# Optimization experiments

Hardware: AMD Instinct MI355X
Metric: run time of the kernel (lower is better)

The kernel has to match this reference:

```python
import jax, jax.numpy as jnp
import numpy as np

FS = 512.0
T = 2048
CYC_PHA, CYC_AMP = 3, 6
NBINS = 18
PHA_BANDS = [(2.0 + 2.0 * k, 4.0 + 2.0 * k) for k in range(10)]
AMP_BANDS = [(30.0 + 12.0 * k, 42.0 + 12.0 * k) for k in range(10)]


def _design_filter(fs, low, high, cycle):
    # windowed-sinc bandpass, taps = cycle * fs / low (tensorpac cycle rule), forced odd
    n = int(cycle * fs / low)
    if n % 2 == 0:
        n += 1
    t = np.arange(n) - (n - 1) / 2.0
    lp = lambda fc: 2.0 * fc / fs * np.sinc(2.0 * fc / fs * t)
    h = (lp(high) - lp(low)) * np.hamming(n)
    fc = 0.5 * (low + high)
    h = h / np.abs(np.sum(h * np.exp(-2j * np.pi * fc / fs * t)))  # unit gain at band center
    return h.astype(np.float32)


def _build_kernels():
    filts = [_design_filter(FS, l, h, CYC_PHA) for l, h in PHA_BANDS] + \
            [_design_filter(FS, l, h, CYC_AMP) for l, h in AMP_BANDS]
    L = max(f.shape[0] for f in filts)
    padded = []
    for f in filts:
        p = L - f.shape[0]
        pl = p // 2
        padded.append(np.pad(f, (pl, p - pl)))
    return np.stack(padded)  # (F, L), L odd


def _conv_same(sig, kernels):
    # sig: (N, Tp), kernels: (F, L) -> (N, F, Tp); cross-correlation, 'same' padding (L odd)
    L = kernels.shape[1]
    pad = (L - 1) // 2
    return jax.lax.conv_general_dilated(
        sig[:, None, :], kernels[:, None, :], window_strides=(1,),
        padding=((pad, L - 1 - pad),), dimension_numbers=("NCH", "OIH", "NCH"))


def _analytic(x):
    # FFT-based Hilbert analytic signal along last axis
    n = x.shape[-1]
    h = np.zeros(n, np.float32)
    h[0] = 1.0
    if n % 2 == 0:
        h[n // 2] = 1.0
        h[1:n // 2] = 2.0
    else:
        h[1:(n + 1) // 2] = 2.0
    return jnp.fft.ifft(jnp.fft.fft(x, axis=-1) * h, axis=-1)


def _modulation_index(pha, amp):
    # Tort MI: pha (B,C,P,S,T), amp (B,C,A,S,T) -> (B,C,P,A)
    idx = jnp.clip(jnp.floor((pha + jnp.pi) / (2.0 * jnp.pi) * NBINS), 0, NBINS - 1).astype(jnp.int32)
    sums, cnts = [], []
    for b in range(NBINS):  # fixed small bin count
        m = (idx == b).astype(amp.dtype)                       # (B,C,P,S,T)
        sums.append(jnp.einsum('bcpst,bcast->bcpas', m, amp))  # (B,C,P,A,S)
        cnts.append(m.sum(-1))                                 # (B,C,P,S)
    amp_sum = jnp.stack(sums, -1)                              # (B,C,P,A,S,N)
    cnt = jnp.stack(cnts, -1)[:, :, :, None, :, :]             # (B,C,P,1,S,N)
    amp_mean = amp_sum / jnp.maximum(cnt, 1.0)
    p = amp_mean / jnp.maximum(amp_mean.sum(-1, keepdims=True), 1e-12)
    log_n = jnp.log(jnp.asarray(NBINS, amp.dtype))
    mi = (log_n + (p * jnp.log(jnp.maximum(p, 1e-12))).sum(-1)) / log_n
    return mi.mean(-1)  # average over segments


def setup_inputs() -> dict:
    key = jax.random.key(0)
    x = jax.random.normal(key, (4, 8, 4, T), dtype=jnp.float32)
    kernels = jnp.asarray(_build_kernels())
    return {"x": x, "kernels": kernels}


def reference(x, kernels):
    B, C, S, Tlen = x.shape
    npha = len(PHA_BANDS)
    pad = kernels.shape[1] - 1  # max_padlen (edge_mode)
    sig = x.reshape(B * C * S, Tlen)
    sig = jnp.pad(sig, ((0, 0), (pad, pad)), mode='reflect')
    # filtfilt_mode: average forward conv and time-reversed conv
    fwd = _conv_same(sig, kernels)
    bwd = _conv_same(sig[:, ::-1], kernels)[:, :, ::-1]
    filt = 0.5 * (fwd + bwd)
    filt = filt[:, :, pad:-pad]  # strip edge padding -> (N, F, T)
    ana = _analytic(filt)
    pha = jnp.arctan2(ana.imag[:, :npha], ana.real[:, :npha])
    amp = jnp.sqrt(ana.real[:, npha:] ** 2 + ana.imag[:, npha:] ** 2)
    pha = pha.reshape(B, C, npha, S, Tlen)
    amp = amp.reshape(B, C, len(AMP_BANDS), S, Tlen)
    return _modulation_index(pha, amp)
```

## Files before the change

kernel.cpp:

```cpp
#include <hip/hip_runtime.h>
#include <math.h>

#define TT 2048
#define LK 769
#define NF 20
#define NS 128
#define NB 18

typedef __attribute__((ext_vector_type(8))) short short8;
typedef __attribute__((ext_vector_type(4))) float f32x4;

__global__ __launch_bounds__(256) void convhil_kernel(const float* __restrict__ x,
                                                      const float* __restrict__ ker,
                                                      float* __restrict__ filt) {
  __shared__ __align__(16) float smem[4400];
  __shared__ int red[4][4];
  __shared__ __align__(16) float2 tw[TT];
  float* w   = smem;
  float* hs1 = smem + 2832;
  float* hs2 = smem + 3616;
  float2* z  = (float2*)smem;
  const int tid = threadIdx.x;
  const int ord = blockIdx.x;
  const int p = ord / NS;
  const int n = ord % NS;
  const int o1 = p;
  const int o2 = 10 + (9 - p);
  const float* xr = x + n * TT;
  for (int j = tid; j < 2832; j += 256) {
    float v = 0.f;
    if (j < 2816) {
      int m = j - 384;
      if (m < 0) m = -m;
      if (m > 2047) m = 4094 - m;
      v = xr[m];
    }
    w[j] = v;
  }
  for (int i = tid; i < TT; i += 256) {
    if (i == 0) { tw[0] = make_float2(1.f, 0.f); }
    else {
      int half = 1 << (31 - __clz(i));
      int j = i - half;
      float ang = -3.14159265358979323846f * (float)j / (float)half;
      float s, c;
      sincosf(ang, &s, &c);
      tw[i] = make_float2(c, s);
    }
  }
  const float* kr1 = ker + o1 * LK;
  const float* kr2 = ker + o2 * LK;
  int k0 = 784, k1 = 0, m0 = 784, m1 = 0;
  for (int k = tid; k < 784; k += 256) {
    float v1 = 0.f, v2 = 0.f;
    if (k < LK) {
      v1 = 0.5f * (kr1[k] + kr1[LK - 1 - k]);
      v2 = 0.5f * (kr2[k] + kr2[LK - 1 - k]);
    }
    hs1[k] = v1;
    hs2[k] = v2;
    if (v1 != 0.f) { k0 = min(k0, k); k1 = max(k1, k + 1); }
    if (v2 != 0.f) { m0 = min(m0, k); m1 = max(m1, k + 1); }
  }
#pragma unroll
  for (int off = 32; off > 0; off >>= 1) {
    k0 = min(k0, __shfl_down(k0, off));
    k1 = max(k1, __shfl_down(k1, off));
    m0 = min(m0, __shfl_down(m0, off));
    m1 = max(m1, __shfl_down(m1, off));
  }
  const int wid = tid >> 6;
  if ((tid & 63) == 0) { red[wid][0] = k0; red[wid][1] = k1; red[wid][2] = m0; red[wid][3] = m1; }
  __syncthreads();
  k0 = min(min(red[0][0], red[1][0]), min(red[2][0], red[3][0]));
  k1 = max(max(red[0][1], red[1][1]), max(red[2][1], red[3][1]));
  m0 = min(min(red[0][2], red[1][2]), min(red[2][2], red[3][2]));
  m1 = max(max(red[0][3], red[1][3]), max(red[2][3], red[3][3]));
  const int A0 = __builtin_amdgcn_readfirstlane(k0 & ~7);
  const int A1 = __builtin_amdgcn_readfirstlane((k1 + 7) & ~7);
  const int B0 = __builtin_amdgcn_readfirstlane(m0 & ~7);
  const int B1 = __builtin_amdgcn_readfirstlane((m1 + 7) & ~7);
  const int U0 = min(A0, B0);
  const int U1 = max(A1, B1);

  const int bA = 4 * tid;
  const int bB = 1024 + 4 * tid;
  float acc1A[4], acc1B[4], acc2A[4], acc2B[4];
#pragma unroll
  for (int r = 0; r < 4; ++r) { acc1A[r] = 0.f; acc1B[r] = 0.f; acc2A[r] = 0.f; acc2B[r] = 0.f; }
  if (U0 < U1) {
    float4 a0 = *(const float4*)&w[bA + U0];
    float4 a1 = *(const float4*)&w[bA + U0 + 4];
    float4 a2 = *(const float4*)&w[bA + U0 + 8];
    float4 b0 = *(const float4*)&w[bB + U0];
    float4 b1 = *(const float4*)&w[bB + U0 + 4];
    float4 b2 = *(const float4*)&w[bB + U0 + 8];
    float4 h1a = *(const float4*)&hs1[U0];
    float4 h1b = *(const float4*)&hs1[U0 + 4];
    float4 h2a = *(const float4*)&hs2[U0];
    float4 h2b = *(const float4*)&hs2[U0 + 4];
    for (int k = U0; k < U1; k += 8) {
      float4 a3 = *(const float4*)&w[bA + k + 12];
      float4 a4 = *(const float4*)&w[bA + k + 16];
      float4 b3 = *(const float4*)&w[bB + k + 12];
      float4 b4 = *(const float4*)&w[bB + k + 16];
      float4 h1an = *(const float4*)&hs1[k + 8];
      float4 h1bn = *(const float4*)&hs1[k + 12];
      float4 h2an = *(const float4*)&hs2[k + 8];
      float4 h2bn = *(const float4*)&hs2[k + 12];
      float wa[11] = {a0.x, a0.y, a0.z, a0.w, a1.x, a1.y, a1.z, a1.w,
                      a2.x, a2.y, a2.z};
      float wb[11] = {b0.x, b0.y, b0.z, b0.w, b1.x, b1.y, b1.z, b1.w,
                      b2.x, b2.y, b2.z};
      float h1[8] = {h1a.x, h1a.y, h1a.z, h1a.w, h1b.x, h1b.y, h1b.z, h1b.w};
      float h2[8] = {h2a.x, h2a.y, h2a.z, h2a.w, h2b.x, h2b.y, h2b.z, h2b.w};
      if (k >= A0 && k < A1) {
#pragma unroll
        for (int r = 0; r < 4; ++r) {
#pragma unroll
          for (int j = 0; j < 8; ++j) {
            acc1A[r] = fmaf(h1[j], wa[r + j], acc1A[r]);
            acc1B[r] = fmaf(h1[j], wb[r + j], acc1B[r]);
          }
        }
      }
      if (k >= B0 && k < B1) {
#pragma unroll
        for (int r = 0; r < 4; ++r) {
#pragma unroll
          for (int j = 0; j < 8; ++j) {
            acc2A[r] = fmaf(h2[j], wa[r + j], acc2A[r]);
            acc2B[r] = fmaf(h2[j], wb[r + j], acc2B[r]);
          }
        }
      }
      a0 = a2; a1 = a3; a2 = a4;
      b0 = b2; b1 = b3; b2 = b4;
      h1a = h1an; h1b = h1bn;
      h2a = h2an; h2b = h2bn;
    }
  }
  __syncthreads();
#pragma unroll
  for (int r = 0; r < 4; ++r) {
    z[bA + r] = make_float2(acc1A[r], acc2A[r]);
    z[bB + r] = make_float2(acc1B[r], acc2B[r]);
  }
  __syncthreads();
  for (int bf = tid; bf < 1024; bf += 256) {
    const float2 t = tw[1024 + bf];
    const float2 u = z[bf];
    const float2 v = z[bf + 1024];
    z[bf] = make_float2(u.x + v.x, u.y + v.y);
    const float dr = u.x - v.x, di = u.y - v.y;
    z[bf + 1024] = make_float2(fmaf(t.x, dr, -(t.y * di)),
                               fmaf(t.x, di, t.y * dr));
  }
  __syncthreads();
  for (int Q = 256; Q >= 1; Q >>= 2) {
    for (int bf = tid; bf < 512; bf += 256) {
      const int j = bf & (Q - 1);
      const int base = ((bf & ~(Q - 1)) << 2) + j;
      const float2 x0 = z[base], x1 = z[base + Q];
      const float2 x2 = z[base + 2 * Q], x3 = z[base + 3 * Q];
      const float2 w1 = tw[2 * Q + j];
      const float2 w2 = tw[Q + j];
      const float w3r = w1.x * w2.x - w1.y * w2.y;
      const float w3i = w1.x * w2.y + w1.y * w2.x;
      const float t0r = x0.x + x2.x, t0i = x0.y + x2.y;
      const float t1r = x0.x - x2.x, t1i = x0.y - x2.y;
      const float t2r = x1.x + x3.x, t2i = x1.y + x3.y;
      const float t3r = x1.x - x3.x, t3i = x1.y - x3.y;
      z[base] = make_float2(t0r + t2r, t0i + t2i);
      const float a1r = t1r + t3i, a1i = t1i - t3r;
      z[base + Q] = make_float2(a1r * w1.x - a1i * w1.y,
                                a1r * w1.y + a1i * w1.x);
      const float a2r = t0r - t2r, a2i = t0i - t2i;
      z[base + 2 * Q] = make_float2(a2r * w2.x - a2i * w2.y,
                                    a2r * w2.y + a2i * w2.x);
      const float a3r = t1r - t3i, a3i = t1i + t3r;
      z[base + 3 * Q] = make_float2(a3r * w3r - a3i * w3i,
                                    a3r * w3i + a3i * w3r);
    }
    __syncthreads();
  }
  for (int pp = tid; pp < TT; pp += 256) {
    if (pp != 0 && pp != 2) {
      if (pp & 2) { z[pp] = make_float2(0.f, 0.f); }
      else        { float2 v = z[pp]; z[pp] = make_float2(2.f * v.x, 2.f * v.y); }
    }
  }
  __syncthreads();
  for (int Q = 1; Q <= 256; Q <<= 2) {
    for (int bf = tid; bf < 512; bf += 256) {
      const int j = bf & (Q - 1);
      const int base = ((bf & ~(Q - 1)) << 2) + j;
      const float2 y0 = z[base], y1 = z[base + Q];
      const float2 y2 = z[base + 2 * Q], y3 = z[base + 3 * Q];
      const float2 w1 = tw[2 * Q + j];
      const float2 w2 = tw[Q + j];
      const float w3r = w1.x * w2.x - w1.y * w2.y;
      const float w3i = w1.x * w2.y + w1.y * w2.x;
      const float u1r = y1.x * w1.x + y1.y * w1.y;
      const float u1i = y1.y * w1.x - y1.x * w1.y;
      const float u2r = y2.x * w2.x + y2.y * w2.y;
      const float u2i = y2.y * w2.x - y2.x * w2.y;
      const float u3r = y3.x * w3r + y3.y * w3i;
      const float u3i = y3.y * w3r - y3.x * w3i;
      const float t0r = y0.x + u2r, t0i = y0.y + u2i;
      const float t1r = y0.x - u2r, t1i = y0.y - u2i;
      const float t2r = u1r + u3r, t2i = u1i + u3i;
      const float t3r = u1r - u3r, t3i = u1i - u3i;
      z[base]         = make_float2(t0r + t2r, t0i + t2i);
      z[base + Q]     = make_float2(t1r - t3i, t1i + t3r);
      z[base + 2 * Q] = make_float2(t0r - t2r, t0i - t2i);
      z[base + 3 * Q] = make_float2(t1r + t3i, t1i - t3r);
    }
    __syncthreads();
  }
  for (int bf = tid; bf < 1024; bf += 256) {
    const float2 t = tw[1024 + bf];
    const float2 u = z[bf];
    const float2 v = z[bf + 1024];
    const float vr = v.x * t.x + v.y * t.y;
    const float vi = v.y * t.x - v.x * t.y;
    z[bf] = make_float2(u.x + vr, u.y + vi);
    z[bf + 1024] = make_float2(u.x - vr, u.y - vi);
  }
  __syncthreads();
  float* out1 = filt + ((size_t)n * NF + o1) * TT;
  float* out2 = filt + ((size_t)n * NF + o2) * TT;
  const float invN = 1.0f / 2048.0f;
  float phA[4], phB[4], amA[4], amB[4];
#pragma unroll
  for (int r = 0; r < 4; ++r) {
    float2 wvA = z[bA + r];
    float h1 = wvA.y * invN - acc2A[r];
    float h2 = acc1A[r] - wvA.x * invN;
    phA[r] = atan2f(h1, acc1A[r]);
    amA[r] = sqrtf(fmaf(acc2A[r], acc2A[r], h2 * h2));
    float2 wvB = z[bB + r];
    float g1 = wvB.y * invN - acc2B[r];
    float g2 = acc1B[r] - wvB.x * invN;
    phB[r] = atan2f(g1, acc1B[r]);
    amB[r] = sqrtf(fmaf(acc2B[r], acc2B[r], g2 * g2));
  }
  *(float4*)&out1[bA] = make_float4(phA[0], phA[1], phA[2], phA[3]);
  *(float4*)&out1[bB] = make_float4(phB[0], phB[1], phB[2], phB[3]);
  *(float4*)&out2[bA] = make_float4(amA[0], amA[1], amA[2], amA[3]);
  *(float4*)&out2[bB] = make_float4(amB[0], amB[1], amB[2], amB[3]);
}

__global__ __launch_bounds__(64) void mi_kernel(const float* __restrict__ filt,
                                                float* __restrict__ mi) {
  __shared__ __align__(16) unsigned int idx32[512];
  __shared__ float Cs[12][19];
  const int lane = threadIdx.x;
  const int blk = blockIdx.x;
  const int bc = blk / 40, jp = blk % 40;
  const float* ph = filt + ((size_t)(bc * 4 + jp / 10) * NF + (jp % 10)) * TT;
  for (int g = lane; g < 512; g += 64) {
    float4 v = *(const float4*)&ph[4 * g];
    float vv[4] = {v.x, v.y, v.z, v.w};
    unsigned int packed = 0;
#pragma unroll
    for (int j = 0; j < 4; ++j) {
      int b = (int)floorf((vv[j] + 3.14159274f) / 6.2831855f * 18.0f);
      b = b < 0 ? 0 : (b > 17 ? 17 : b);
      packed |= ((unsigned int)b) << (8 * j);
    }
    idx32[g] = packed;
  }
  __syncthreads();
  const int n16 = lane & 15;
  const int quad = lane >> 4;
  const int aband = n16 < 10 ? n16 : 9;
  const int ja = (jp & 3) + 4 * aband;
  const float* aptr = filt + ((size_t)(bc * 4 + ja / 10) * NF + 10 + (ja % 10)) * TT
                      + quad * 8;
  const bool isAmp = (n16 < 10);
  const bool isOne = (n16 == 10);
  f32x4 acc0 = {0.f, 0.f, 0.f, 0.f};
  f32x4 acc1 = {0.f, 0.f, 0.f, 0.f};
  float4 p0 = *(const float4*)(aptr);
  float4 p1 = *(const float4*)(aptr + 4);
  for (int s = 0; s < 64; ++s) {
    float4 c0 = p0, c1 = p1;
    if (s < 63) {
      p0 = *(const float4*)(aptr + (s + 1) * 32);
      p1 = *(const float4*)(aptr + (s + 1) * 32 + 4);
    }
    float a[8] = {c0.x, c0.y, c0.z, c0.w, c1.x, c1.y, c1.z, c1.w};
    short8 ah, am_, al;
#pragma unroll
    for (int j = 0; j < 8; ++j) {
      float v = isAmp ? a[j] : (isOne ? 1.0f : 0.0f);
      unsigned int u = __float_as_uint(v);
      float h = __uint_as_float(u & 0xFFFF0000u);
      float r1 = v - h;
      unsigned int u2 = __float_as_uint(r1);
      float md = __uint_as_float(u2 & 0xFFFF0000u);
      float r2 = r1 - md;
      unsigned int u3 = __float_as_uint(r2);
      ah[j] = (short)(u >> 16);
      am_[j] = (short)(u2 >> 16);
      al[j] = (short)(u3 >> 16);
    }
    const int dw = s * 8 + quad * 2;
    unsigned int d0 = idx32[dw], d1 = idx32[dw + 1];
    short8 b0, b1;
#pragma unroll
    for (int j = 0; j < 8; ++j) {
      unsigned int byte = ((j < 4 ? d0 : d1) >> ((j & 3) * 8)) & 0xFFu;
      b0[j] = (byte == (unsigned int)n16) ? (short)0x3F80 : (short)0;
      b1[j] = (byte == (unsigned int)(n16 + 16)) ? (short)0x3F80 : (short)0;
    }
    acc0 = __builtin_amdgcn_mfma_f32_16x16x32_bf16(ah, b0, acc0, 0, 0, 0);
    acc0 = __builtin_amdgcn_mfma_f32_16x16x32_bf16(am_, b0, acc0, 0, 0, 0);
    acc0 = __builtin_amdgcn_mfma_f32_16x16x32_bf16(al, b0, acc0, 0, 0, 0);
    acc1 = __builtin_amdgcn_mfma_f32_16x16x32_bf16(ah, b1, acc1, 0, 0, 0);
    acc1 = __builtin_amdgcn_mfma_f32_16x16x32_bf16(am_, b1, acc1, 0, 0, 0);
    acc1 = __builtin_amdgcn_mfma_f32_16x16x32_bf16(al, b1, acc1, 0, 0, 0);
  }
#pragma unroll
  for (int r = 0; r < 4; ++r) {
    int row = quad * 4 + r;
    if (row < 11) {
      Cs[row][n16] = acc0[r];
      if (n16 < 2) Cs[row][16 + n16] = acc1[r];
    }
  }
  __syncthreads();
  if (lane < 10) {
    float tot = 0.f, mb_[18];
#pragma unroll
    for (int b = 0; b < 18; ++b) {
      float mb = Cs[lane][b] / fmaxf(Cs[10][b], 1.0f);
      mb_[b] = mb; tot += mb;
    }
    tot = fmaxf(tot, 1e-12f);
    float s = 0.f;
#pragma unroll
    for (int b = 0; b < 18; ++b) {
      float pb = mb_[b] / tot;
      s += pb * logf(fmaxf(pb, 1e-12f));
    }
    const float LOGN = 2.8903717578961645f;
    mi[(size_t)blk * 10 + lane] = (LOGN + s) / LOGN;
  }
}

__global__ void out_kernel(const float* __restrict__ mi, float* __restrict__ out) {
  int i = blockIdx.x * 256 + threadIdx.x;
  if (i < 3200) {
    int a = i % 10, p = (i / 10) % 10, bc = i / 100;
    float s = 0.f;
    for (int sp = 0; sp < 4; ++sp)
      s += mi[((size_t)(bc * 40 + p * 4 + sp)) * 10 + a];
    out[i] = 0.25f * s;
  }
}

extern "C" void kernel_launch(void* const* d_in, const int* in_sizes, int n_in,
                              void* d_out, int out_size, void* d_ws, size_t ws_size,
                              hipStream_t stream) {
  (void)in_sizes; (void)n_in; (void)out_size; (void)ws_size;
  const float* x = (const float*)d_in[0];
  const float* ker = (const float*)d_in[1];
  float* out = (float*)d_out;
  float* filt = (float*)d_ws;
  float* mi = filt + (size_t)NS * NF * TT;

  convhil_kernel<<<NS * 10, 256, 0, stream>>>(x, ker, filt);
  mi_kernel<<<32 * 40, 64, 0, stream>>>(filt, mi);
  out_kernel<<<(3200 + 255) / 256, 256, 0, stream>>>(mi, out);
}
```

Baseline: 151.6 us.

## Precompute twiddles and symmetric filters once; split MI accumulation across four waves

A new prep kernel computes the FFT twiddle table, the symmetrized filter taps and their nonzero ranges once, instead of every convhil block redoing sincos, the filter folding and a block reduction. As a result convhil no longer holds the twiddle table in LDS, which frees about 16 KB of shared memory per block. It now reads twiddles from global memory, which adds global/L2 traffic inside the FFT. The MI kernel grows from one wave to four waves per block, each accumulating a quarter of the time segments, with partial histograms combined in LDS. The extra kernel launch adds a small fixed cost.

After: 139.4 us. 1.09x faster.

```diff
diff --git a/kernel.cpp b/kernel.cpp
--- a/kernel.cpp
+++ b/kernel.cpp
@@ -10,12 +10,56 @@
 typedef __attribute__((ext_vector_type(8))) short short8;
 typedef __attribute__((ext_vector_type(4))) float f32x4;
 
+__global__ __launch_bounds__(256) void prep_kernel(const float* __restrict__ ker,
+                                                   float2* __restrict__ tw,
+                                                   float* __restrict__ hsym,
+                                                   int* __restrict__ rng) {
+  __shared__ int red[4][2];
+  const int blk = blockIdx.x;
+  const int tid = threadIdx.x;
+  if (blk < 8) {
+    int i = blk * 256 + tid;
+    if (i == 0) { tw[0] = make_float2(1.f, 0.f); }
+    else {
+      int half = 1 << (31 - __clz(i));
+      int j = i - half;
+      float ang = -3.14159265358979323846f * (float)j / (float)half;
+      float s, c;
+      sincosf(ang, &s, &c);
+      tw[i] = make_float2(c, s);
+    }
+    return;
+  }
+  const int o = blk - 8;
+  const float* kr = ker + o * LK;
+  int k0 = 784, k1 = 0;
+  for (int k = tid; k < 784; k += 256) {
+    float v = 0.f;
+    if (k < LK) v = 0.5f * (kr[k] + kr[LK - 1 - k]);
+    hsym[o * 784 + k] = v;
+    if (v != 0.f) { k0 = min(k0, k); k1 = max(k1, k + 1); }
+  }
+#pragma unroll
+  for (int off = 32; off > 0; off >>= 1) {
+    k0 = min(k0, __shfl_down(k0, off));
+    k1 = max(k1, __shfl_down(k1, off));
+  }
+  if ((tid & 63) == 0) { red[tid >> 6][0] = k0; red[tid >> 6][1] = k1; }
+  __syncthreads();
+  if (tid == 0) {
+    k0 = min(min(red[0][0], red[1][0]), min(red[2][0], red[3][0]));
+    k1 = max(max(red[0][1], red[1][1]), max(red[2][1], red[3][1]));
+    rng[2 * o] = k0 & ~7;
+    rng[2 * o + 1] = (k1 + 7) & ~7;
+  }
+}
+
 __global__ __launch_bounds__(256) void convhil_kernel(const float* __restrict__ x,
-                                                      const float* __restrict__ ker,
+                                                      const float* __restrict__ hsym,
+                                                      const int* __restrict__ rng,
+                                                      const float2* __restrict__ tw,
                                                       float* __restrict__ filt) {
   __shared__ __align__(16) float smem[4400];
-  __shared__ int red[4][4];
-  __shared__ __align__(16) float2 tw[TT];
   float* w   = smem;
   float* hs1 = smem + 2832;
   float* hs2 = smem + 3616;
@@ -37,51 +81,17 @@
     }
     w[j] = v;
   }
-  for (int i = tid; i < TT; i += 256) {
-    if (i == 0) { tw[0] = make_float2(1.f, 0.f); }
-    else {
-      int half = 1 << (31 - __clz(i));
-      int j = i - half;
-      float ang = -3.14159265358979323846f * (float)j / (float)half;
-      float s, c;
-      sincosf(ang, &s, &c);
-      tw[i] = make_float2(c, s);
-    }
-  }
-  const float* kr1 = ker + o1 * LK;
-  const float* kr2 = ker + o2 * LK;
-  int k0 = 784, k1 = 0, m0 = 784, m1 = 0;
+  const float* h1g = hsym + o1 * 784;
+  const float* h2g = hsym + o2 * 784;
   for (int k = tid; k < 784; k += 256) {
-    float v1 = 0.f, v2 = 0.f;
-    if (k < LK) {
-      v1 = 0.5f * (kr1[k] + kr1[LK - 1 - k]);
-      v2 = 0.5f * (kr2[k] + kr2[LK - 1 - k]);
-    }
-    hs1[k] = v1;
-    hs2[k] = v2;
-    if (v1 != 0.f) { k0 = min(k0, k); k1 = max(k1, k + 1); }
-    if (v2 != 0.f) { m0 = min(m0, k); m1 = max(m1, k + 1); }
-  }
-#pragma unroll
-  for (int off = 32; off > 0; off >>= 1) {
-    k0 = min(k0, __shfl_down(k0, off));
-    k1 = max(k1, __shfl_down(k1, off));
-    m0 = min(m0, __shfl_down(m0, off));
-    m1 = max(m1, __shfl_down(m1, off));
-  }
-  const int wid = tid >> 6;
-  if ((tid & 63) == 0) { red[wid][0] = k0; red[wid][1] = k1; red[wid][2] = m0; red[wid][3] = m1; }
-  __syncthreads();
-  k0 = min(min(red[0][0], red[1][0]), min(red[2][0], red[3][0]));
-  k1 = max(max(red[0][1], red[1][1]), max(red[2][1], red[3][1]));
-  m0 = min(min(red[0][2], red[1][2]), min(red[2][2], red[3][2]));
-  m1 = max(max(red[0][3], red[1][3]), max(red[2][3], red[3][3]));
-  const int A0 = __builtin_amdgcn_readfirstlane(k0 & ~7);
-  const int A1 = __builtin_amdgcn_readfirstlane((k1 + 7) & ~7);
-  const int B0 = __builtin_amdgcn_readfirstlane(m0 & ~7);
-  const int B1 = __builtin_amdgcn_readfirstlane((m1 + 7) & ~7);
+    hs1[k] = h1g[k];
+    hs2[k] = h2g[k];
+  }
+  const int A0 = rng[2 * o1], A1 = rng[2 * o1 + 1];
+  const int B0 = rng[2 * o2], B1 = rng[2 * o2 + 1];
   const int U0 = min(A0, B0);
   const int U1 = max(A1, B1);
+  __syncthreads();
 
   const int bA = 4 * tid;
   const int bB = 1024 + 4 * tid;
@@ -251,15 +261,17 @@
   *(float4*)&out2[bB] = make_float4(amB[0], amB[1], amB[2], amB[3]);
 }
 
-__global__ __launch_bounds__(64) void mi_kernel(const float* __restrict__ filt,
-                                                float* __restrict__ mi) {
+__global__ __launch_bounds__(256) void mi_kernel(const float* __restrict__ filt,
+                                                 float* __restrict__ mi) {
   __shared__ __align__(16) unsigned int idx32[512];
-  __shared__ float Cs[12][19];
-  const int lane = threadIdx.x;
+  __shared__ float Cp[4][12][19];
+  const int tid = threadIdx.x;
+  const int wave = tid >> 6;
+  const int lane = tid & 63;
   const int blk = blockIdx.x;
   const int bc = blk / 40, jp = blk % 40;
   const float* ph = filt + ((size_t)(bc * 4 + jp / 10) * NF + (jp % 10)) * TT;
-  for (int g = lane; g < 512; g += 64) {
+  for (int g = tid; g < 512; g += 256) {
     float4 v = *(const float4*)&ph[4 * g];
     float vv[4] = {v.x, v.y, v.z, v.w};
     unsigned int packed = 0;
@@ -282,11 +294,12 @@
   const bool isOne = (n16 == 10);
   f32x4 acc0 = {0.f, 0.f, 0.f, 0.f};
   f32x4 acc1 = {0.f, 0.f, 0.f, 0.f};
-  float4 p0 = *(const float4*)(aptr);
-  float4 p1 = *(const float4*)(aptr + 4);
-  for (int s = 0; s < 64; ++s) {
+  const int s0 = wave * 16, s1 = s0 + 16;
+  float4 p0 = *(const float4*)(aptr + s0 * 32);
+  float4 p1 = *(const float4*)(aptr + s0 * 32 + 4);
+  for (int s = s0; s < s1; ++s) {
     float4 c0 = p0, c1 = p1;
-    if (s < 63) {
+    if (s < s1 - 1) {
       p0 = *(const float4*)(aptr + (s + 1) * 32);
       p1 = *(const float4*)(aptr + (s + 1) * 32 + 4);
     }
@@ -326,16 +339,18 @@
   for (int r = 0; r < 4; ++r) {
     int row = quad * 4 + r;
     if (row < 11) {
-      Cs[row][n16] = acc0[r];
-      if (n16 < 2) Cs[row][16 + n16] = acc1[r];
-    }
-  }
-  __syncthreads();
-  if (lane < 10) {
+      Cp[wave][row][n16] = acc0[r];
+      if (n16 < 2) Cp[wave][row][16 + n16] = acc1[r];
+    }
+  }
+  __syncthreads();
+  if (tid < 10) {
     float tot = 0.f, mb_[18];
 #pragma unroll
     for (int b = 0; b < 18; ++b) {
-      float mb = Cs[lane][b] / fmaxf(Cs[10][b], 1.0f);
+      float s = Cp[0][tid][b] + Cp[1][tid][b] + Cp[2][tid][b] + Cp[3][tid][b];
+      float c = Cp[0][10][b] + Cp[1][10][b] + Cp[2][10][b] + Cp[3][10][b];
+      float mb = s / fmaxf(c, 1.0f);
       mb_[b] = mb; tot += mb;
     }
     tot = fmaxf(tot, 1e-12f);
@@ -346,7 +361,7 @@
       s += pb * logf(fmaxf(pb, 1e-12f));
     }
     const float LOGN = 2.8903717578961645f;
-    mi[(size_t)blk * 10 + lane] = (LOGN + s) / LOGN;
+    mi[(size_t)blk * 10 + tid] = (LOGN + s) / LOGN;
   }
 }
 
@@ -370,8 +385,12 @@
   float* out = (float*)d_out;
   float* filt = (float*)d_ws;
   float* mi = filt + (size_t)NS * NF * TT;
-
-  convhil_kernel<<<NS * 10, 256, 0, stream>>>(x, ker, filt);
-  mi_kernel<<<32 * 40, 64, 0, stream>>>(filt, mi);
+  float2* tw = (float2*)(mi + 12800);
+  float* hsym = (float*)(tw + TT);
+  int* rng = (int*)(hsym + NF * 784);
+
+  prep_kernel<<<28, 256, 0, stream>>>(ker, tw, hsym, rng);
+  convhil_kernel<<<NS * 10, 256, 0, stream>>>(x, hsym, rng, tw, filt);
+  mi_kernel<<<32 * 40, 256, 0, stream>>>(filt, mi);
   out_kernel<<<(3200 + 255) / 256, 256, 0, stream>>>(mi, out);
 }
```
